# Kernel optimization log

Hardware: AMD Instinct MI355X
Metric: run time of the kernel (lower is better)

Reference implementation:

```python
import jax, jax.numpy as jnp
import numpy as np
from jax import lax

B, NL, W = 1024, 64, 2048
EPS_N = 1e-8   # added to n in m12 denominator (as in torch source)
EPS_Y = 1e-9   # added to E before admittance division (as in torch source)


def setup_inputs() -> dict:
    key = jax.random.key(0)
    k1, k2 = jax.random.split(key)
    # refractive indices of typical dielectrics, thicknesses ~quarter-wave in nm
    n_layers = 1.0 + 1.5 * jax.random.uniform(k1, (B, NL), dtype=jnp.float32)
    d_layers = 20.0 + 200.0 * jax.random.uniform(k2, (B, NL), dtype=jnp.float32)
    wavelengths = jnp.linspace(400.0, 800.0, W, dtype=jnp.float32)
    return {"n_layers": n_layers, "d_layers": d_layers, "wavelengths": wavelengths}


def reference(n_layers, d_layers, wavelengths):
    # n_layers: (B, N) real -> complex64; d_layers: (B, N) nm; wavelengths: (W,) nm
    n = n_layers.astype(jnp.complex64)
    k0 = (2.0 * np.pi / wavelengths).astype(jnp.complex64)  # (W,)
    num_layers = n.shape[1]

    def step(M, nd):
        # M: (B, W, 2, 2) complex64 running product; nd = (n_i, d_i) each (B,)
        n_i, d_i = nd
        phi = n_i[:, None] * d_i[:, None] * k0[None, :]          # (B, W)
        c = jnp.cos(phi)
        s = jnp.sin(phi)
        m12 = -1j * s / (n_i[:, None] + EPS_N)
        m21 = -1j * n_i[:, None] * s
        # layer characteristic matrix (B, W, 2, 2)
        M_layer = jnp.stack(
            [jnp.stack([c, m12], axis=-1), jnp.stack([m21, c], axis=-1)],
            axis=-2,
        )
        M_new = jnp.einsum("bwij,bwjk->bwik", M, M_layer)
        return M_new, None

    M0 = jnp.broadcast_to(
        jnp.eye(2, dtype=jnp.complex64), (n.shape[0], k0.shape[0], 2, 2)
    )
    # scan over interior layers 1 .. N-2 (substrate/ambient are semi-infinite)
    xs = (n[:, 1 : num_layers - 1].T, d_layers[:, 1 : num_layers - 1].T)
    M, _ = lax.scan(step, M0, xs)

    n_in = n[:, 0]    # (B,) incident-side index
    n_sub = n[:, -1]  # (B,) substrate index
    # EH = M @ [1, n_sub]^T  ->  E, H : (B, W)
    E = M[..., 0, 0] + M[..., 0, 1] * n_sub[:, None]
    H = M[..., 1, 0] + M[..., 1, 1] * n_sub[:, None]
    Y = H / (E + EPS_Y)
    r = (n_in[:, None] - Y) / (n_in[:, None] + Y)
    R = jnp.abs(r) ** 2
    return R.astype(jnp.float32)
```

## Files before the change

### kernel.cpp

```cpp
#include <hip/hip_runtime.h>
#include <math.h>

constexpr int B  = 1024;
constexpr int NL = 64;
constexpr int W  = 2048;
constexpr int INNER = NL - 2;
constexpr float EPS_N = 1e-8f;
constexpr float EPS_Y = 1e-9f;


__global__ __launch_bounds__(64)
void prep_kernel(const float* __restrict__ n_layers,
                 const float* __restrict__ d_layers,
                 float4* __restrict__ ws)
{
    const int b = blockIdx.x;
    const int i = threadIdx.x;
    if (i < INNER) {
        const float n = n_layers[b * NL + 1 + i];
        const float d = d_layers[b * NL + 1 + i];
        ws[b * 64 + i] = make_float4(n * d, n, 1.0f / (n + EPS_N), 0.0f);
    } else if (i == INNER) {
        ws[b * 64 + INNER] =
            make_float4(n_layers[b * NL], n_layers[b * NL + NL - 1], 0.0f, 0.0f);
    }
}

__global__ __launch_bounds__(256)
void tmm_kernel(const float4* __restrict__ lw,
                const float* __restrict__ wavelengths,
                float* __restrict__ out)
{
    const int b   = blockIdx.y;
    const int tid = threadIdx.x;
    const int w0  = blockIdx.x * 1024 + tid * 4;
    const float4* __restrict__ Lb = lw + b * 64;

    const float4 wl = *(const float4*)&wavelengths[w0];
    const float il0 = 1.0f / wl.x;
    const float il1 = 1.0f / wl.y;
    const float il2 = 1.0f / wl.z;
    const float il3 = 1.0f / wl.w;

    float a0 = 1.f, bb0 = 0.f, cc0 = 0.f, dd0 = 1.f;
    float a1 = 1.f, bb1 = 0.f, cc1 = 0.f, dd1 = 1.f;
    float a2 = 1.f, bb2 = 0.f, cc2 = 0.f, dd2 = 1.f;
    float a3 = 1.f, bb3 = 0.f, cc3 = 0.f, dd3 = 1.f;

#define STEP(k)                                                     \
    {                                                               \
        const float ph = L.x * il##k;            \
        const float s  = __builtin_amdgcn_sinf(ph);                 \
        const float c  = __builtin_amdgcn_cosf(ph);                 \
        const float ns = L.y * s;                \
        const float sn = L.z * s;                \
        const float an = fmaf(bb##k,  ns, a##k  * c);               \
        const float bn = fmaf(a##k,  -sn, bb##k * c);               \
        const float cn = fmaf(dd##k, -ns, cc##k * c);               \
        const float dn = fmaf(cc##k,  sn, dd##k * c);               \
        a##k = an; bb##k = bn; cc##k = cn; dd##k = dn;              \
    }

    #pragma unroll
    for (int i = 0; i < INNER; ++i) {
        const float4 L = Lb[i];
        STEP(0)
        STEP(1)
        STEP(2)
        STEP(3)
    }
#undef STEP

    const float4 Eg  = Lb[INNER];
    const float n_in  = Eg.x;
    const float n_sub = Eg.y;

    float4 R;
#define EPI(k, slot)                                                \
    {                                                               \
        const float Er = a##k + EPS_Y;                              \
        const float Ei = bb##k * n_sub;                             \
        const float Hr = dd##k * n_sub;                             \
        const float Hi = cc##k;                                     \
        const float Nr = fmaf(n_in, Er, -Hr);                       \
        const float Ni = fmaf(n_in, Ei, -Hi);                       \
        const float Dr = fmaf(n_in, Er,  Hr);                       \
        const float Di = fmaf(n_in, Ei,  Hi);                       \
        slot = (Nr * Nr + Ni * Ni) / (Dr * Dr + Di * Di);           \
    }
    EPI(0, R.x)
    EPI(1, R.y)
    EPI(2, R.z)
    EPI(3, R.w)
#undef EPI

    *(float4*)&out[b * W + w0] = R;
}

extern "C" void kernel_launch(void* const* d_in, const int* in_sizes, int n_in,
                              void* d_out, int out_size, void* d_ws, size_t ws_size,
                              hipStream_t stream)
{
    const float* n_layers    = (const float*)d_in[0];
    const float* d_layers    = (const float*)d_in[1];
    const float* wavelengths = (const float*)d_in[2];
    float* out = (float*)d_out;
    float4* ws = (float4*)d_ws;

    prep_kernel<<<dim3(B), dim3(64), 0, stream>>>(n_layers, d_layers, ws);

    dim3 grid(W / 1024, B);
    dim3 block(256);
    tmm_kernel<<<grid, block, 0, stream>>>(ws, wavelengths, out);
}
```

Before: 99.19 us.

## Fuse layer preprocessing into main kernel via per-lane loads and readlane broadcast

Drops the separate prep kernel and its workspace round trip. Each wavefront lane now loads one layer's n and d, computes n*d and 1/(n+eps) itself, and the layer loop broadcasts them with readlane instead of loading a float4 per layer from memory. This removes a kernel launch and the per-iteration scalar/vector loads, but every block redoes the small per-layer prep and the readlane calls add scalar instructions to the unrolled loop.

```diff
diff --git a/kernel.cpp b/kernel.cpp
--- a/kernel.cpp
+++ b/kernel.cpp
@@ -9,32 +9,26 @@
 constexpr float EPS_Y = 1e-9f;
 
 
-__global__ __launch_bounds__(64)
-void prep_kernel(const float* __restrict__ n_layers,
-                 const float* __restrict__ d_layers,
-                 float4* __restrict__ ws)
+static __device__ __forceinline__ float bcast_lane(float v, int lane)
 {
-    const int b = blockIdx.x;
-    const int i = threadIdx.x;
-    if (i < INNER) {
-        const float n = n_layers[b * NL + 1 + i];
-        const float d = d_layers[b * NL + 1 + i];
-        ws[b * 64 + i] = make_float4(n * d, n, 1.0f / (n + EPS_N), 0.0f);
-    } else if (i == INNER) {
-        ws[b * 64 + INNER] =
-            make_float4(n_layers[b * NL], n_layers[b * NL + NL - 1], 0.0f, 0.0f);
-    }
+    return __uint_as_float(__builtin_amdgcn_readlane(__float_as_uint(v), lane));
 }
 
 __global__ __launch_bounds__(256)
-void tmm_kernel(const float4* __restrict__ lw,
+void tmm_kernel(const float* __restrict__ n_layers,
+                const float* __restrict__ d_layers,
                 const float* __restrict__ wavelengths,
                 float* __restrict__ out)
 {
-    const int b   = blockIdx.y;
-    const int tid = threadIdx.x;
-    const int w0  = blockIdx.x * 1024 + tid * 4;
-    const float4* __restrict__ Lb = lw + b * 64;
+    const int b    = blockIdx.y;
+    const int tid  = threadIdx.x;
+    const int lane = tid & 63;
+    const int w0   = blockIdx.x * 1024 + tid * 4;
+
+    const float n_l  = n_layers[b * NL + lane];
+    const float d_l  = d_layers[b * NL + lane];
+    const float nd_l = n_l * d_l;
+    const float rc_l = 1.0f / (n_l + EPS_N);
 
     const float4 wl = *(const float4*)&wavelengths[w0];
     const float il0 = 1.0f / wl.x;
@@ -49,11 +43,11 @@
 
 #define STEP(k)                                                     \
     {                                                               \
-        const float ph = L.x * il##k;            \
+        const float ph = nd * il##k;               \
         const float s  = __builtin_amdgcn_sinf(ph);                 \
         const float c  = __builtin_amdgcn_cosf(ph);                 \
-        const float ns = L.y * s;                \
-        const float sn = L.z * s;                \
+        const float ns = nn * s;                   \
+        const float sn = rc * s;                   \
         const float an = fmaf(bb##k,  ns, a##k  * c);               \
         const float bn = fmaf(a##k,  -sn, bb##k * c);               \
         const float cn = fmaf(dd##k, -ns, cc##k * c);               \
@@ -63,7 +57,9 @@
 
     #pragma unroll
     for (int i = 0; i < INNER; ++i) {
-        const float4 L = Lb[i];
+        const float nd = bcast_lane(nd_l, i + 1);
+        const float nn = bcast_lane(n_l,  i + 1);
+        const float rc = bcast_lane(rc_l, i + 1);
         STEP(0)
         STEP(1)
         STEP(2)
@@ -71,9 +67,8 @@
     }
 #undef STEP
 
-    const float4 Eg  = Lb[INNER];
-    const float n_in  = Eg.x;
-    const float n_sub = Eg.y;
+    const float n_in  = bcast_lane(n_l, 0);
+    const float n_sub = bcast_lane(n_l, NL - 1);
 
     float4 R;
 #define EPI(k, slot)                                                \
@@ -105,11 +100,8 @@
     const float* d_layers    = (const float*)d_in[1];
     const float* wavelengths = (const float*)d_in[2];
     float* out = (float*)d_out;
-    float4* ws = (float4*)d_ws;
-
-    prep_kernel<<<dim3(B), dim3(64), 0, stream>>>(n_layers, d_layers, ws);
 
     dim3 grid(W / 1024, B);
     dim3 block(256);
-    tmm_kernel<<<grid, block, 0, stream>>>(ws, wavelengths, out);
+    tmm_kernel<<<grid, block, 0, stream>>>(n_layers, d_layers, wavelengths, out);
 }
```

Result: no change. 98.21 us (-1.0%).
